# Kernel tuning notes

Hardware: AMD Instinct MI355X
Metric: run time of the kernel (lower is better)

The kernel has to match this reference:

```python
import jax, jax.numpy as jnp
import numpy as np

N, E, D, H, G, C = 100000, 1200000, 64, 64, 128, 10


def setup_inputs() -> dict:
    key = jax.random.key(0)
    ks = jax.random.split(key, 20)
    def lin(k, fin, fout):
        kw, kb = jax.random.split(k)
        s = 1.0 / np.sqrt(fin)
        return (jax.random.uniform(kw, (fin, fout), jnp.float32, -s, s),
                jax.random.uniform(kb, (fout,), jnp.float32, -s, s))
    w1a, b1a = lin(ks[0], D, H)
    w1b, b1b = lin(ks[1], H, H)
    w2a, b2a = lin(ks[2], H, H)
    w2b, b2b = lin(ks[3], H, H)
    w3a, b3a = lin(ks[4], H, H)
    w3b, b3b = lin(ks[5], H, H)
    wc, bc = lin(ks[6], H, C)
    x = jax.random.normal(ks[7], (N, D), jnp.float32)
    edge_index = jax.random.randint(ks[8], (2, E), 0, N, dtype=jnp.int32)
    batch = jnp.sort(jax.random.randint(ks[9], (N,), 0, G, dtype=jnp.int32))
    return {"x": x, "w1a": w1a, "b1a": b1a, "w1b": w1b, "b1b": b1b,
            "w2a": w2a, "b2a": b2a, "w2b": w2b, "b2b": b2b,
            "w3a": w3a, "b3a": b3a, "w3b": w3b, "b3b": b3b,
            "wc": wc, "bc": bc, "edge_index": edge_index, "batch": batch}


def _gin_layer(x, src, dst, wa, ba, wb, bb):
    # GINConv (eps=0): mlp(x + sum_{j in N(i)} x_j), then outer ReLU from GIN.forward
    agg = jax.ops.segment_sum(x[src], dst, num_segments=N)  # [N, d]
    h = x + agg
    h = jax.nn.relu(h @ wa + ba) @ wb + bb
    return jax.nn.relu(h)


def reference(x, w1a, b1a, w1b, b1b, w2a, b2a, w2b, b2b,
              w3a, b3a, w3b, b3b, wc, bc, edge_index, batch):
    src, dst = edge_index[0], edge_index[1]
    x = _gin_layer(x, src, dst, w1a, b1a, w1b, b1b)
    x = _gin_layer(x, src, dst, w2a, b2a, w2b, b2b)
    x = _gin_layer(x, src, dst, w3a, b3a, w3b, b3b)
    # global mean pool over graphs
    sums = jax.ops.segment_sum(x, batch, num_segments=G)              # [G, H]
    cnts = jax.ops.segment_sum(jnp.ones((N,), x.dtype), batch, num_segments=G)
    pooled = sums / jnp.maximum(cnts, 1.0)[:, None]
    return pooled @ wc + bc  # [G, C]
```

## Files before the change

### kernel.cpp

```cpp
#include <hip/hip_runtime.h>
#include <hip/hip_bf16.h>


#define N_NODES 100000
#define N_EDGES 1200000
#define N_GRAPH 128
#define N_CLS   10
#define NBUCK   391
#define BCAP    4096
#define BSH     12
#define NTILES  6250

typedef __bf16 bf16_t;
typedef __bf16 bf16x8 __attribute__((ext_vector_type(8)));
typedef float  f32x4  __attribute__((ext_vector_type(4)));

__global__ void tobf_kernel(const float* __restrict__ x, bf16_t* __restrict__ xb,
                            int* __restrict__ bcnt, float* __restrict__ gsum,
                            const float* __restrict__ w1a, const float* __restrict__ w1b,
                            const float* __restrict__ w2a, const float* __restrict__ w2b,
                            const float* __restrict__ w3a, const float* __restrict__ w3b,
                            bf16_t* __restrict__ wfragG,
                            bf16_t* __restrict__ hPad, bf16_t* __restrict__ xAPad) {
    const int tid = threadIdx.x;
    if (blockIdx.x == 0) {
        for (int i = tid; i < NBUCK; i += 256) bcnt[i] = 0;
    } else if (blockIdx.x == 1) {
        f32x4* g4 = (f32x4*)gsum;
        for (int i = tid; i < N_GRAPH * 16; i += 256)
            g4[i] = (f32x4){0.f, 0.f, 0.f, 0.f};
        if (tid < 64) {
            xb[N_NODES * 64 + tid]    = (bf16_t)0.f;
            hPad[N_NODES * 64 + tid]  = (bf16_t)0.f;
            xAPad[N_NODES * 64 + tid] = (bf16_t)0.f;
        }
    } else if (blockIdx.x <= 4) {
        const int L = blockIdx.x - 2;
        const float* wA = L == 0 ? w1a : (L == 1 ? w2a : w3a);
        const float* wB = L == 0 ? w1b : (L == 1 ? w2b : w3b);
        const int k  = tid >> 2;
        const int n0 = (tid & 3) << 4;
        const int ks = k >> 5, qd = (k >> 3) & 3, jj = k & 7;
        const int fi = ((n0 >> 4) << 1) + ks;
#pragma unroll
        for (int m = 0; m < 2; ++m) {
            const float* w = m ? wB : wA;
            const f32x4 v0 = *(const f32x4*)(w + k * 64 + n0);
            const f32x4 v1 = *(const f32x4*)(w + k * 64 + n0 + 4);
            const f32x4 v2 = *(const f32x4*)(w + k * 64 + n0 + 8);
            const f32x4 v3 = *(const f32x4*)(w + k * 64 + n0 + 12);
            bf16_t* dst = wfragG + ((L * 2 + m) * 8 + fi) * 512 + jj;
#pragma unroll
            for (int l = 0; l < 4; ++l) {
                dst[(qd * 16 + l) * 8]      = (bf16_t)v0[l];
                dst[(qd * 16 + 4 + l) * 8]  = (bf16_t)v1[l];
                dst[(qd * 16 + 8 + l) * 8]  = (bf16_t)v2[l];
                dst[(qd * 16 + 12 + l) * 8] = (bf16_t)v3[l];
            }
        }
    }
    const int i = (blockIdx.x * 256 + tid) * 8;
    const f32x4 a = *(const f32x4*)(x + i);
    const f32x4 b = *(const f32x4*)(x + i + 4);
    bf16x8 o;
#pragma unroll
    for (int j = 0; j < 4; ++j) { o[j] = (bf16_t)a[j]; o[4 + j] = (bf16_t)b[j]; }
    *(bf16x8*)(xb + i) = o;
}

__global__ void binA_kernel(const int* __restrict__ ei,
                            int* __restrict__ bcnt,
                            int* __restrict__ bpair) {
    __shared__ int lcnt[NBUCK];
    __shared__ int lbase[NBUCK];
    const int t = threadIdx.x;
    for (int b = t; b < NBUCK; b += 512) lcnt[b] = 0;
    __syncthreads();
    const int e0 = (blockIdx.x * 512 + t) * 4;
    int4 s4, d4; int b[4], r[4];
    const bool valid = e0 < N_EDGES;
    if (valid) {
        s4 = *(const int4*)(ei + e0);
        d4 = *(const int4*)(ei + N_EDGES + e0);
        b[0] = d4.x >> 8; b[1] = d4.y >> 8; b[2] = d4.z >> 8; b[3] = d4.w >> 8;
        r[0] = atomicAdd(&lcnt[b[0]], 1);
        r[1] = atomicAdd(&lcnt[b[1]], 1);
        r[2] = atomicAdd(&lcnt[b[2]], 1);
        r[3] = atomicAdd(&lcnt[b[3]], 1);
    }
    __syncthreads();
    for (int bb = t; bb < NBUCK; bb += 512) {
        const int c = lcnt[bb];
        lbase[bb] = c ? atomicAdd(&bcnt[bb], c) : 0;
    }
    __syncthreads();
    if (valid) {
        const int ss[4] = {s4.x, s4.y, s4.z, s4.w};
        const int dd[4] = {d4.x, d4.y, d4.z, d4.w};
#pragma unroll
        for (int j = 0; j < 4; ++j) {
            const int slot = lbase[b[j]] + r[j];
            if (slot < BCAP)
                bpair[(b[j] << BSH) + slot] = (ss[j] << 8) | (dd[j] & 255);
        }
    }
}

__global__ void sortfill_kernel(const int* __restrict__ bpair,
                                const int* __restrict__ bcnt,
                                int* __restrict__ offset, int* __restrict__ csr) {
    __shared__ int red[512];
    __shared__ int hist[256];
    __shared__ int l[256];
    __shared__ int cursor[256];
    const int b = blockIdx.x;
    const int t = threadIdx.x;
    const int base = b << BSH;

    int part = 0;
    for (int i = t; i < b; i += 512) {
        int c = bcnt[i];
        part += (c < BCAP ? c : BCAP);
    }
    red[t] = part;
    __syncthreads();
    for (int d = 256; d > 0; d >>= 1) {
        if (t < d) red[t] += red[t + d];
        __syncthreads();
    }
    const int cbase = red[0];
    int cnt = bcnt[b];
    cnt = cnt < BCAP ? cnt : BCAP;
    if (b == NBUCK - 1 && t == 0) offset[N_NODES] = cbase + cnt;
    __syncthreads();

    if (t < 256) hist[t] = 0;
    __syncthreads();
    for (int i = t; i < cnt; i += 512)
        atomicAdd(&hist[bpair[base + i] & 255], 1);
    __syncthreads();

    int v = 0;
    if (t < 256) { v = hist[t]; l[t] = v; }
    __syncthreads();
    for (int d = 1; d < 256; d <<= 1) {
        int u = 0;
        if (t < 256) { u = l[t]; if (t >= d) u += l[t - d]; }
        __syncthreads();
        if (t < 256) l[t] = u;
        __syncthreads();
    }
    if (t < 256) {
        const int gpos = cbase + l[t] - v;
        const int node = (b << 8) + t;
        if (node < N_NODES) offset[node] = gpos;
        cursor[t] = gpos;
    }
    __syncthreads();

    for (int i = t; i < cnt; i += 512) {
        const int p = bpair[base + i];
        const int pos = atomicAdd(&cursor[p & 255], 1);
        csr[pos] = p >> 8;
    }
}

#define G8(S, J, ACC)                                                          \
    {                                                                          \
        const int t0 = __shfl(S, (J) + 0), t1 = __shfl(S, (J) + 1);            \
        const int t2 = __shfl(S, (J) + 2), t3 = __shfl(S, (J) + 3);            \
        const int t4 = __shfl(S, (J) + 4), t5 = __shfl(S, (J) + 5);            \
        const int t6 = __shfl(S, (J) + 6), t7 = __shfl(S, (J) + 7);            \
        const float u0 = (float)x[t0 * 64 + f], u1 = (float)x[t1 * 64 + f];    \
        const float u2 = (float)x[t2 * 64 + f], u3 = (float)x[t3 * 64 + f];    \
        const float u4 = (float)x[t4 * 64 + f], u5 = (float)x[t5 * 64 + f];    \
        const float u6 = (float)x[t6 * 64 + f], u7 = (float)x[t7 * 64 + f];    \
        ACC += ((u0 + u1) + (u2 + u3)) + ((u4 + u5) + (u6 + u7));              \
    }

#define ROWPAIR(I, SA, CA, DA, OA, SB, CB, DB, OB)                             \
    {                                                                          \
        float accA = (float)x[(r0w + I) * 64 + f];                             \
        float accB = (float)x[(r0w + I + 4) * 64 + f];                         \
        const int cmax = (CA) > (CB) ? (CA) : (CB);                            \
        for (int j = 0; j < cmax; j += 8) {                                    \
            if (j < (CA)) { G8(SA, j, accA) }                                  \
            if (j < (CB)) { G8(SB, j, accB) }                                  \
        }                                                                      \
        if ((DA) > 64 || (DB) > 64) {                      \
            for (int base = 64; base < (DA) || base < (DB); base += 64) {      \
                const int ra = (DA) - base, rb2 = (DB) - base;                 \
                const int ca2 = ra <= 0 ? 0 : (ra < 64 ? ra : 64);             \
                const int cb2 = rb2 <= 0 ? 0 : (rb2 < 64 ? rb2 : 64);          \
                int sA2 = N_NODES, sB2 = N_NODES;                              \
                if (f < ca2) sA2 = csr[(OA) + base + f];                       \
                if (f < cb2) sB2 = csr[(OB) + base + f];                       \
                const int cm2 = ca2 > cb2 ? ca2 : cb2;                         \
                for (int j = 0; j < cm2; j += 8) {                             \
                    if (j < ca2) { G8(sA2, j, accA) }                          \
                    if (j < cb2) { G8(sB2, j, accB) }                          \
                }                                                              \
            }                                                                  \
        }                                                                      \
        hs[half * 8 + I][lane]     = (bf16_t)accA;                             \
        hs[half * 8 + I + 4][lane] = (bf16_t)accB;                             \
    }

template <int POOL>
__global__ void gmlp_kernel(const bf16_t* __restrict__ x,
                            const int* __restrict__ offset,
                            const int* __restrict__ csr,
                            const bf16_t* __restrict__ wf,
                            const float* __restrict__ ba, const float* __restrict__ bb,
                            bf16_t* __restrict__ xout,
                            const int* __restrict__ batch,
                            float* __restrict__ gsum) {
    __shared__ __align__(16) bf16_t hs[16][72];
    __shared__ __align__(16) bf16_t h2[16][72];

    const int tid  = threadIdx.x;
    const int half = tid >> 6;
    const int lane = tid & 63;
    const int l15  = lane & 15;
    const int quad = lane >> 4;

    const int rb  = blockIdx.x * 16;
    const int r0w = rb + half * 8;
    const int f   = lane;

    int offv = 0;
    if (lane < 9) offv = offset[r0w + lane];
    const int o0 = __shfl(offv, 0), o1 = __shfl(offv, 1), o2 = __shfl(offv, 2);
    const int o3 = __shfl(offv, 3), o4 = __shfl(offv, 4), o5 = __shfl(offv, 5);
    const int o6 = __shfl(offv, 6), o7 = __shfl(offv, 7), o8 = __shfl(offv, 8);
    const int d0 = o1 - o0, d1 = o2 - o1, d2 = o3 - o2, d3 = o4 - o3;
    const int d4 = o5 - o4, d5 = o6 - o5, d6 = o7 - o6, d7 = o8 - o7;
    const int c0 = d0 < 64 ? d0 : 64, c1 = d1 < 64 ? d1 : 64;
    const int c2 = d2 < 64 ? d2 : 64, c3 = d3 < 64 ? d3 : 64;
    const int c4 = d4 < 64 ? d4 : 64, c5 = d5 < 64 ? d5 : 64;
    const int c6 = d6 < 64 ? d6 : 64, c7 = d7 < 64 ? d7 : 64;

    int s0 = N_NODES, s1 = N_NODES, s2 = N_NODES, s3 = N_NODES;
    int s4 = N_NODES, s5 = N_NODES, s6 = N_NODES, s7 = N_NODES;
    if (f < c0) s0 = csr[o0 + f];
    if (f < c1) s1 = csr[o1 + f];
    if (f < c2) s2 = csr[o2 + f];
    if (f < c3) s3 = csr[o3 + f];
    if (f < c4) s4 = csr[o4 + f];
    if (f < c5) s5 = csr[o5 + f];
    if (f < c6) s6 = csr[o6 + f];
    if (f < c7) s7 = csr[o7 + f];

    ROWPAIR(0, s0, c0, d0, o0, s4, c4, d4, o4)
    ROWPAIR(1, s1, c1, d1, o1, s5, c5, d5, o5)
    ROWPAIR(2, s2, c2, d2, o2, s6, c6, d6, o6)
    ROWPAIR(3, s3, c3, d3, o3, s7, c7, d7, o7)

    __syncthreads();

    {
        bf16x8 af[2];
#pragma unroll
        for (int ks = 0; ks < 2; ++ks)
            af[ks] = *(const bf16x8*)(&hs[l15][ks * 32 + quad * 8]);
#pragma unroll
        for (int c = 0; c < 2; ++c) {
            const int ct = half * 2 + c;
            const bf16x8 b0 = *(const bf16x8*)(wf + (0 * 8 + ct * 2 + 0) * 512 + lane * 8);
            const bf16x8 b1 = *(const bf16x8*)(wf + (0 * 8 + ct * 2 + 1) * 512 + lane * 8);
            f32x4 acc = {0.f, 0.f, 0.f, 0.f};
            acc = __builtin_amdgcn_mfma_f32_16x16x32_bf16(af[0], b0, acc, 0, 0, 0);
            acc = __builtin_amdgcn_mfma_f32_16x16x32_bf16(af[1], b1, acc, 0, 0, 0);
            const float bv = ba[ct * 16 + l15];
#pragma unroll
            for (int r = 0; r < 4; ++r) {
                float h = acc[r] + bv;
                h = h > 0.f ? h : 0.f;
                h2[quad * 4 + r][ct * 16 + l15] = (bf16_t)h;
            }
        }
    }

    __syncthreads();

    {
        bf16x8 a2[2];
#pragma unroll
        for (int ks = 0; ks < 2; ++ks)
            a2[ks] = *(const bf16x8*)(&h2[l15][ks * 32 + quad * 8]);
#pragma unroll
        for (int c = 0; c < 2; ++c) {
            const int ct = half * 2 + c;
            const bf16x8 b0 = *(const bf16x8*)(wf + (1 * 8 + ct * 2 + 0) * 512 + lane * 8);
            const bf16x8 b1 = *(const bf16x8*)(wf + (1 * 8 + ct * 2 + 1) * 512 + lane * 8);
            f32x4 acc = {0.f, 0.f, 0.f, 0.f};
            acc = __builtin_amdgcn_mfma_f32_16x16x32_bf16(a2[0], b0, acc, 0, 0, 0);
            acc = __builtin_amdgcn_mfma_f32_16x16x32_bf16(a2[1], b1, acc, 0, 0, 0);
            const float bv = bb[ct * 16 + l15];
#pragma unroll
            for (int r = 0; r < 4; ++r) {
                float h = acc[r] + bv;
                h = h > 0.f ? h : 0.f;
                hs[quad * 4 + r][ct * 16 + l15] = (bf16_t)h;
            }
        }
    }

    __syncthreads();

    if (POOL) {
        int cur = -1;
        float acc = 0.f;
        for (int r = 0; r < 8; ++r) {
            const int row = r0w + r;
            const int g = batch[row];
            const float v = (float)hs[half * 8 + r][lane];
            if (g != cur) {
                if (cur >= 0) unsafeAtomicAdd(gsum + cur * 64 + lane, acc);
                acc = 0.f;
                cur = g;
            }
            acc += v;
        }
        if (cur >= 0) unsafeAtomicAdd(gsum + cur * 64 + lane, acc);
    } else {
        const int row16 = half * 8 + (lane >> 3);
        const int colg  = (lane & 7) * 8;
        const bf16x8 v = *(const bf16x8*)&hs[row16][colg];
        *(bf16x8*)(xout + (rb + row16) * 64 + colg) = v;
    }
}

__global__ void cls_kernel(const float* __restrict__ gsum,
                           const int* __restrict__ batch,
                           const float* __restrict__ wc, const float* __restrict__ bc,
                           float* __restrict__ out) {
    const int g = blockIdx.x;
    const int c = threadIdx.x;
    if (c >= N_CLS) return;
    int lo = 0, hi = N_NODES;
    while (lo < hi) { const int m = (lo + hi) >> 1; if (batch[m] < g) lo = m + 1; else hi = m; }
    const int lb = lo;
    lo = 0; hi = N_NODES;
    while (lo < hi) { const int m = (lo + hi) >> 1; if (batch[m] <= g) lo = m + 1; else hi = m; }
    const int cnt = lo - lb;
    const float inv = 1.f / (float)(cnt > 1 ? cnt : 1);
    float acc = bc[c];
    for (int k = 0; k < 64; ++k)
        acc += gsum[g * 64 + k] * inv * wc[k * N_CLS + c];
    out[g * N_CLS + c] = acc;
}

extern "C" void kernel_launch(void* const* d_in, const int* in_sizes, int n_in,
                              void* d_out, int out_size, void* d_ws, size_t ws_size,
                              hipStream_t stream) {
    const float* x   = (const float*)d_in[0];
    const float* w1a = (const float*)d_in[1];
    const float* b1a = (const float*)d_in[2];
    const float* w1b = (const float*)d_in[3];
    const float* b1b = (const float*)d_in[4];
    const float* w2a = (const float*)d_in[5];
    const float* b2a = (const float*)d_in[6];
    const float* w2b = (const float*)d_in[7];
    const float* b2b = (const float*)d_in[8];
    const float* w3a = (const float*)d_in[9];
    const float* b3a = (const float*)d_in[10];
    const float* w3b = (const float*)d_in[11];
    const float* b3b = (const float*)d_in[12];
    const float* wc  = (const float*)d_in[13];
    const float* bc  = (const float*)d_in[14];
    const int*   ei    = (const int*)d_in[15];
    const int*   batch = (const int*)d_in[16];
    float* out = (float*)d_out;

    char*   ws     = (char*)d_ws;
    int*    bcnt   = (int*)ws;
    int*    offset = (int*)(ws + 3136);
    int*    csr    = (int*)(ws + 403152);
    int*    bpair  = (int*)(ws + 5203152);
    bf16_t* xbf    = (bf16_t*)(ws + 11609296);
    bf16_t* h      = (bf16_t*)(ws + 24409424);
    bf16_t* xA     = (bf16_t*)(ws + 37209552);
    float*  gsum   = (float*)(ws + 50009680);
    bf16_t* wfragG = (bf16_t*)(ws + 50042448);

    const int e4grid = (N_EDGES / 4 + 511) / 512;

    tobf_kernel<<<(N_NODES * 64) / (256 * 8), 256, 0, stream>>>(
        x, xbf, bcnt, gsum, w1a, w1b, w2a, w2b, w3a, w3b, wfragG, h, xA);

    binA_kernel<<<e4grid, 512, 0, stream>>>(ei, bcnt, bpair);
    sortfill_kernel<<<NBUCK, 512, 0, stream>>>(bpair, bcnt, offset, csr);

    gmlp_kernel<0><<<NTILES, 128, 0, stream>>>(xbf, offset, csr, wfragG,         b1a, b1b, xA, nullptr, nullptr);
    gmlp_kernel<0><<<NTILES, 128, 0, stream>>>(xA,  offset, csr, wfragG + 8192,  b2a, b2b, h,  nullptr, nullptr);
    gmlp_kernel<1><<<NTILES, 128, 0, stream>>>(h,   offset, csr, wfragG + 16384, b3a, b3b, nullptr, batch, gsum);

    cls_kernel<<<N_GRAPH, 64, 0, stream>>>(gsum, batch, wc, bc, out);
}
```

Measured before the change: 269.3 us.

## Fuse bf16 conversion with edge binning and make MLP tiles per-wave

The x-to-bf16 conversion, weight-fragment setup and edge bucketing are merged into one prep kernel with 512-thread blocks. The bucket-counter reset moves to a hipMemsetAsync. sortfill now runs with 1024 threads per block. In the GIN MLP kernel each wave gets its own 16x72 shared tiles, handles its 8 rows and computes all four output column tiles, which removes the block-wide __syncthreads. In exchange each wave issues twice as many MFMAs, half of them on unused padding rows, and the change saves one kernel launch.

```diff
diff --git a/kernel.cpp b/kernel.cpp
--- a/kernel.cpp
+++ b/kernel.cpp
@@ -10,32 +10,71 @@
 #define BCAP    4096
 #define BSH     12
 #define NTILES  6250
+#define TOBF_BLKS 1563
+#define BINA_BLKS 586
 
 typedef __bf16 bf16_t;
 typedef __bf16 bf16x8 __attribute__((ext_vector_type(8)));
 typedef float  f32x4  __attribute__((ext_vector_type(4)));
 
-__global__ void tobf_kernel(const float* __restrict__ x, bf16_t* __restrict__ xb,
+__global__ void prep_kernel(const float* __restrict__ x, bf16_t* __restrict__ xb,
                             int* __restrict__ bcnt, float* __restrict__ gsum,
                             const float* __restrict__ w1a, const float* __restrict__ w1b,
                             const float* __restrict__ w2a, const float* __restrict__ w2b,
                             const float* __restrict__ w3a, const float* __restrict__ w3b,
                             bf16_t* __restrict__ wfragG,
-                            bf16_t* __restrict__ hPad, bf16_t* __restrict__ xAPad) {
+                            bf16_t* __restrict__ hPad, bf16_t* __restrict__ xAPad,
+                            const int* __restrict__ ei, int* __restrict__ bpair) {
+    __shared__ int lcnt[NBUCK];
+    __shared__ int lbase[NBUCK];
     const int tid = threadIdx.x;
-    if (blockIdx.x == 0) {
-        for (int i = tid; i < NBUCK; i += 256) bcnt[i] = 0;
-    } else if (blockIdx.x == 1) {
+    const int blk = blockIdx.x;
+
+    if (blk >= TOBF_BLKS) {
+        for (int b = tid; b < NBUCK; b += 512) lcnt[b] = 0;
+        __syncthreads();
+        const int e0 = ((blk - TOBF_BLKS) * 512 + tid) * 4;
+        int4 s4, d4; int b[4], r[4];
+        const bool valid = e0 < N_EDGES;
+        if (valid) {
+            s4 = *(const int4*)(ei + e0);
+            d4 = *(const int4*)(ei + N_EDGES + e0);
+            b[0] = d4.x >> 8; b[1] = d4.y >> 8; b[2] = d4.z >> 8; b[3] = d4.w >> 8;
+            r[0] = atomicAdd(&lcnt[b[0]], 1);
+            r[1] = atomicAdd(&lcnt[b[1]], 1);
+            r[2] = atomicAdd(&lcnt[b[2]], 1);
+            r[3] = atomicAdd(&lcnt[b[3]], 1);
+        }
+        __syncthreads();
+        for (int bb = tid; bb < NBUCK; bb += 512) {
+            const int c = lcnt[bb];
+            lbase[bb] = c ? atomicAdd(&bcnt[bb], c) : 0;
+        }
+        __syncthreads();
+        if (valid) {
+            const int ss[4] = {s4.x, s4.y, s4.z, s4.w};
+            const int dd[4] = {d4.x, d4.y, d4.z, d4.w};
+#pragma unroll
+            for (int j = 0; j < 4; ++j) {
+                const int slot = lbase[b[j]] + r[j];
+                if (slot < BCAP)
+                    bpair[(b[j] << BSH) + slot] = (ss[j] << 8) | (dd[j] & 255);
+            }
+        }
+        return;
+    }
+
+    if (blk == 0) {
         f32x4* g4 = (f32x4*)gsum;
-        for (int i = tid; i < N_GRAPH * 16; i += 256)
+        for (int i = tid; i < N_GRAPH * 16; i += 512)
             g4[i] = (f32x4){0.f, 0.f, 0.f, 0.f};
         if (tid < 64) {
             xb[N_NODES * 64 + tid]    = (bf16_t)0.f;
             hPad[N_NODES * 64 + tid]  = (bf16_t)0.f;
             xAPad[N_NODES * 64 + tid] = (bf16_t)0.f;
         }
-    } else if (blockIdx.x <= 4) {
-        const int L = blockIdx.x - 2;
+    } else if (blk <= 3 && tid < 256) {
+        const int L = blk - 1;
         const float* wA = L == 0 ? w1a : (L == 1 ? w2a : w3a);
         const float* wB = L == 0 ? w1b : (L == 1 ? w2b : w3b);
         const int k  = tid >> 2;
@@ -59,57 +98,22 @@
             }
         }
     }
-    const int i = (blockIdx.x * 256 + tid) * 8;
-    const f32x4 a = *(const f32x4*)(x + i);
-    const f32x4 b = *(const f32x4*)(x + i + 4);
-    bf16x8 o;
-#pragma unroll
-    for (int j = 0; j < 4; ++j) { o[j] = (bf16_t)a[j]; o[4 + j] = (bf16_t)b[j]; }
-    *(bf16x8*)(xb + i) = o;
-}
-
-__global__ void binA_kernel(const int* __restrict__ ei,
-                            int* __restrict__ bcnt,
-                            int* __restrict__ bpair) {
-    __shared__ int lcnt[NBUCK];
-    __shared__ int lbase[NBUCK];
-    const int t = threadIdx.x;
-    for (int b = t; b < NBUCK; b += 512) lcnt[b] = 0;
-    __syncthreads();
-    const int e0 = (blockIdx.x * 512 + t) * 4;
-    int4 s4, d4; int b[4], r[4];
-    const bool valid = e0 < N_EDGES;
-    if (valid) {
-        s4 = *(const int4*)(ei + e0);
-        d4 = *(const int4*)(ei + N_EDGES + e0);
-        b[0] = d4.x >> 8; b[1] = d4.y >> 8; b[2] = d4.z >> 8; b[3] = d4.w >> 8;
-        r[0] = atomicAdd(&lcnt[b[0]], 1);
-        r[1] = atomicAdd(&lcnt[b[1]], 1);
-        r[2] = atomicAdd(&lcnt[b[2]], 1);
-        r[3] = atomicAdd(&lcnt[b[3]], 1);
-    }
-    __syncthreads();
-    for (int bb = t; bb < NBUCK; bb += 512) {
-        const int c = lcnt[bb];
-        lbase[bb] = c ? atomicAdd(&bcnt[bb], c) : 0;
-    }
-    __syncthreads();
-    if (valid) {
-        const int ss[4] = {s4.x, s4.y, s4.z, s4.w};
-        const int dd[4] = {d4.x, d4.y, d4.z, d4.w};
-#pragma unroll
-        for (int j = 0; j < 4; ++j) {
-            const int slot = lbase[b[j]] + r[j];
-            if (slot < BCAP)
-                bpair[(b[j] << BSH) + slot] = (ss[j] << 8) | (dd[j] & 255);
-        }
+
+    const int i = (blk * 512 + tid) * 8;
+    if (i < N_NODES * 64) {
+        const f32x4 a = *(const f32x4*)(x + i);
+        const f32x4 b = *(const f32x4*)(x + i + 4);
+        bf16x8 o;
+#pragma unroll
+        for (int j = 0; j < 4; ++j) { o[j] = (bf16_t)a[j]; o[4 + j] = (bf16_t)b[j]; }
+        *(bf16x8*)(xb + i) = o;
     }
 }
 
 __global__ void sortfill_kernel(const int* __restrict__ bpair,
                                 const int* __restrict__ bcnt,
                                 int* __restrict__ offset, int* __restrict__ csr) {
-    __shared__ int red[512];
+    __shared__ int red[1024];
     __shared__ int hist[256];
     __shared__ int l[256];
     __shared__ int cursor[256];
@@ -118,13 +122,13 @@
     const int base = b << BSH;
 
     int part = 0;
-    for (int i = t; i < b; i += 512) {
+    for (int i = t; i < b; i += 1024) {
         int c = bcnt[i];
         part += (c < BCAP ? c : BCAP);
     }
     red[t] = part;
     __syncthreads();
-    for (int d = 256; d > 0; d >>= 1) {
+    for (int d = 512; d > 0; d >>= 1) {
         if (t < d) red[t] += red[t + d];
         __syncthreads();
     }
@@ -136,7 +140,7 @@
 
     if (t < 256) hist[t] = 0;
     __syncthreads();
-    for (int i = t; i < cnt; i += 512)
+    for (int i = t; i < cnt; i += 1024)
         atomicAdd(&hist[bpair[base + i] & 255], 1);
     __syncthreads();
 
@@ -158,7 +162,7 @@
     }
     __syncthreads();
 
-    for (int i = t; i < cnt; i += 512) {
+    for (int i = t; i < cnt; i += 1024) {
         const int p = bpair[base + i];
         const int pos = atomicAdd(&cursor[p & 255], 1);
         csr[pos] = p >> 8;
@@ -202,8 +206,8 @@
                 }                                                              \
             }                                                                  \
         }                                                                      \
-        hs[half * 8 + I][lane]     = (bf16_t)accA;                             \
-        hs[half * 8 + I + 4][lane] = (bf16_t)accB;                             \
+        hsw[half][I][lane]     = (bf16_t)accA;                                 \
+        hsw[half][I + 4][lane] = (bf16_t)accB;                                 \
     }
 
 template <int POOL>
@@ -215,8 +219,8 @@
                             bf16_t* __restrict__ xout,
                             const int* __restrict__ batch,
                             float* __restrict__ gsum) {
-    __shared__ __align__(16) bf16_t hs[16][72];
-    __shared__ __align__(16) bf16_t h2[16][72];
+    __shared__ __align__(16) bf16_t hsw[2][16][72];
+    __shared__ __align__(16) bf16_t h2w[2][16][72];
 
     const int tid  = threadIdx.x;
     const int half = tid >> 6;
@@ -224,8 +228,7 @@
     const int l15  = lane & 15;
     const int quad = lane >> 4;
 
-    const int rb  = blockIdx.x * 16;
-    const int r0w = rb + half * 8;
+    const int r0w = blockIdx.x * 16 + half * 8;
     const int f   = lane;
 
     int offv = 0;
@@ -256,16 +259,13 @@
     ROWPAIR(2, s2, c2, d2, o2, s6, c6, d6, o6)
     ROWPAIR(3, s3, c3, d3, o3, s7, c7, d7, o7)
 
-    __syncthreads();
-
     {
         bf16x8 af[2];
 #pragma unroll
         for (int ks = 0; ks < 2; ++ks)
-            af[ks] = *(const bf16x8*)(&hs[l15][ks * 32 + quad * 8]);
-#pragma unroll
-        for (int c = 0; c < 2; ++c) {
-            const int ct = half * 2 + c;
+            af[ks] = *(const bf16x8*)(&hsw[half][l15][ks * 32 + quad * 8]);
+#pragma unroll
+        for (int ct = 0; ct < 4; ++ct) {
             const bf16x8 b0 = *(const bf16x8*)(wf + (0 * 8 + ct * 2 + 0) * 512 + lane * 8);
             const bf16x8 b1 = *(const bf16x8*)(wf + (0 * 8 + ct * 2 + 1) * 512 + lane * 8);
             f32x4 acc = {0.f, 0.f, 0.f, 0.f};
@@ -276,21 +276,18 @@
             for (int r = 0; r < 4; ++r) {
                 float h = acc[r] + bv;
                 h = h > 0.f ? h : 0.f;
-                h2[quad * 4 + r][ct * 16 + l15] = (bf16_t)h;
-            }
-        }
-    }
-
-    __syncthreads();
+                h2w[half][quad * 4 + r][ct * 16 + l15] = (bf16_t)h;
+            }
+        }
+    }
 
     {
         bf16x8 a2[2];
 #pragma unroll
         for (int ks = 0; ks < 2; ++ks)
-            a2[ks] = *(const bf16x8*)(&h2[l15][ks * 32 + quad * 8]);
-#pragma unroll
-        for (int c = 0; c < 2; ++c) {
-            const int ct = half * 2 + c;
+            a2[ks] = *(const bf16x8*)(&h2w[half][l15][ks * 32 + quad * 8]);
+#pragma unroll
+        for (int ct = 0; ct < 4; ++ct) {
             const bf16x8 b0 = *(const bf16x8*)(wf + (1 * 8 + ct * 2 + 0) * 512 + lane * 8);
             const bf16x8 b1 = *(const bf16x8*)(wf + (1 * 8 + ct * 2 + 1) * 512 + lane * 8);
             f32x4 acc = {0.f, 0.f, 0.f, 0.f};
@@ -301,12 +298,10 @@
             for (int r = 0; r < 4; ++r) {
                 float h = acc[r] + bv;
                 h = h > 0.f ? h : 0.f;
-                hs[quad * 4 + r][ct * 16 + l15] = (bf16_t)h;
-            }
-        }
-    }
-
-    __syncthreads();
+                hsw[half][quad * 4 + r][ct * 16 + l15] = (bf16_t)h;
+            }
+        }
+    }
 
     if (POOL) {
         int cur = -1;
@@ -314,7 +309,7 @@
         for (int r = 0; r < 8; ++r) {
             const int row = r0w + r;
             const int g = batch[row];
-            const float v = (float)hs[half * 8 + r][lane];
+            const float v = (float)hsw[half][r][lane];
             if (g != cur) {
                 if (cur >= 0) unsafeAtomicAdd(gsum + cur * 64 + lane, acc);
                 acc = 0.f;
@@ -324,10 +319,10 @@
         }
         if (cur >= 0) unsafeAtomicAdd(gsum + cur * 64 + lane, acc);
     } else {
-        const int row16 = half * 8 + (lane >> 3);
-        const int colg  = (lane & 7) * 8;
-        const bf16x8 v = *(const bf16x8*)&hs[row16][colg];
-        *(bf16x8*)(xout + (rb + row16) * 64 + colg) = v;
+        const int row8 = lane >> 3;
+        const int colg = (lane & 7) * 8;
+        const bf16x8 v = *(const bf16x8*)&hsw[half][row8][colg];
+        *(bf16x8*)(xout + (r0w + row8) * 64 + colg) = v;
     }
 }
 
@@ -384,13 +379,12 @@
     float*  gsum   = (float*)(ws + 50009680);
     bf16_t* wfragG = (bf16_t*)(ws + 50042448);
 
-    const int e4grid = (N_EDGES / 4 + 511) / 512;
-
-    tobf_kernel<<<(N_NODES * 64) / (256 * 8), 256, 0, stream>>>(
-        x, xbf, bcnt, gsum, w1a, w1b, w2a, w2b, w3a, w3b, wfragG, h, xA);
-
-    binA_kernel<<<e4grid, 512, 0, stream>>>(ei, bcnt, bpair);
-    sortfill_kernel<<<NBUCK, 512, 0, stream>>>(bpair, bcnt, offset, csr);
+    hipMemsetAsync(bcnt, 0, NBUCK * sizeof(int), stream);
+
+    prep_kernel<<<TOBF_BLKS + BINA_BLKS, 512, 0, stream>>>(
+        x, xbf, bcnt, gsum, w1a, w1b, w2a, w2b, w3a, w3b, wfragG, h, xA, ei, bpair);
+
+    sortfill_kernel<<<NBUCK, 1024, 0, stream>>>(bpair, bcnt, offset, csr);
 
     gmlp_kernel<0><<<NTILES, 128, 0, stream>>>(xbf, offset, csr, wfragG,         b1a, b1b, xA, nullptr, nullptr);
     gmlp_kernel<0><<<NTILES, 128, 0, stream>>>(xA,  offset, csr, wfragG + 8192,  b2a, b2b, h,  nullptr, nullptr);
```

Measured after the change: 269.4 us. About the same (+0.0%).
